# Optimization experiments

Measured on AMD Instinct MI355X. Metric: run time of the kernel, lower is better.

The kernel has to match this reference:

```python
import jax, jax.numpy as jnp
import numpy as np

B, N, K = 8, 1024, 16        # graphs, points per graph, kNN fan-in (loop=True includes self)
LATENT = 256
EPS = 1e-5                   # PyG BatchNorm eps


def _bn(x, g, b):
    # training-mode batch norm over all leading (node/edge) dims, per channel
    ax = tuple(range(x.ndim - 1))
    mu = jnp.mean(x, axis=ax, keepdims=True)
    var = jnp.var(x, axis=ax, keepdims=True)
    return g * (x - mu) * jax.lax.rsqrt(var + EPS) + b


def setup_inputs() -> dict:
    key = jax.random.key(0)
    ks = jax.random.split(key, 12)

    def lin(k, fi, fo):
        s = (6.0 / (fi + fo)) ** 0.5
        kw, kb = jax.random.split(k)
        W = jax.random.uniform(kw, (fi, fo), jnp.float32, -s, s)
        bb = jax.random.uniform(kb, (fo,), jnp.float32, -s, s)
        return W, bb

    pos = jax.random.normal(ks[0], (B * N, 3), jnp.float32)
    batch = jnp.repeat(jnp.arange(B, dtype=jnp.int32), N)

    c1_W1, c1_b1 = lin(ks[1], 6, 64)
    c1_W2, c1_b2 = lin(ks[2], 64, 64)
    c2_W1, c2_b1 = lin(ks[3], 67, 64)
    c2_W2, c2_b2 = lin(ks[4], 64, 128)
    c2_W3, c2_b3 = lin(ks[5], 128, 1024)
    lin_W, lin_b = lin(ks[6], 1024, LATENT)

    return {
        "pos": pos, "batch": batch,
        "c1_W1": c1_W1, "c1_b1": c1_b1,
        "c1_g1": jnp.ones((64,), jnp.float32), "c1_be1": jnp.zeros((64,), jnp.float32),
        "c1_W2": c1_W2, "c1_b2": c1_b2,
        "c2_W1": c2_W1, "c2_b1": c2_b1,
        "c2_g1": jnp.ones((64,), jnp.float32), "c2_be1": jnp.zeros((64,), jnp.float32),
        "c2_W2": c2_W2, "c2_b2": c2_b2,
        "c2_g2": jnp.ones((128,), jnp.float32), "c2_be2": jnp.zeros((128,), jnp.float32),
        "c2_W3": c2_W3, "c2_b3": c2_b3,
        "lin_W": lin_W, "lin_b": lin_b,
        "lin_g": jnp.ones((LATENT,), jnp.float32), "lin_be": jnp.zeros((LATENT,), jnp.float32),
    }


def reference(pos, batch,
              c1_W1, c1_b1, c1_g1, c1_be1, c1_W2, c1_b2,
              c2_W1, c2_b1, c2_g1, c2_be1, c2_W2, c2_b2,
              c2_g2, c2_be2, c2_W3, c2_b3,
              lin_W, lin_b, lin_g, lin_be):
    # ---- kNN graph (per-graph, loop=True: self is nearest) ----
    p3 = pos.reshape(B, N, 3)
    sq = jnp.sum(p3 * p3, axis=-1)                                   # [B,N]
    d = sq[:, :, None] + sq[:, None, :] - 2.0 * jnp.einsum('bnd,bmd->bnm', p3, p3)
    _, nbr = jax.lax.top_k(-d, K)                                    # [B,N,K] neighbor ids
    idx = (nbr + (jnp.arange(B) * N)[:, None, None]).reshape(B * N, K)

    # ---- PointNetConv 1: gather -> MLP([6,64,64]) -> max aggregate ----
    pj = pos[idx]                                                    # [P,K,3]
    rel = pj - pos[:, None, :]                                       # [P,K,3]
    feat = jnp.concatenate([pj, rel], axis=-1)                       # [P,K,6]
    h = jax.nn.relu(_bn(feat @ c1_W1 + c1_b1, c1_g1, c1_be1))
    x1 = jnp.max(h @ c1_W2 + c1_b2, axis=1)                          # [P,64]

    # ---- PointNetConv 2: MLP([67,64,128,1024]) -> max aggregate ----
    feat2 = jnp.concatenate([x1[idx], rel], axis=-1)                 # [P,K,67]
    h = jax.nn.relu(_bn(feat2 @ c2_W1 + c2_b1, c2_g1, c2_be1))
    h = jax.nn.relu(_bn(h @ c2_W2 + c2_b2, c2_g2, c2_be2))
    x2 = jnp.max(h @ c2_W3 + c2_b3, axis=1)                          # [P,1024]

    # ---- global max pool per graph + final MLP (plain_last=False) ----
    g = x2.reshape(B, N, -1).max(axis=1)                             # [B,1024]
    return jax.nn.relu(_bn(g @ lin_W + lin_b, lin_g, lin_be))        # [B,LATENT]
```

## Files before the change

### kernel.cpp

```cpp
#include <hip/hip_runtime.h>
#include <math.h>

#define NB   8
#define NPTS 1024
#define PTS  8192
#define KNN  16
#define PK   (PTS*KNN)

typedef __attribute__((ext_vector_type(8))) _Float16 f16x8;
typedef __attribute__((ext_vector_type(4))) float f32x4;

__device__ __forceinline__ unsigned short f2h(float f) {
  _Float16 h = (_Float16)f;
  union { _Float16 h; unsigned short u; } c; c.h = h;
  return c.u;
}
__device__ __forceinline__ float h2f(unsigned short u) {
  union { unsigned short u; _Float16 h; } c; c.u = u;
  return (float)c.h;
}

__global__ __launch_bounds__(256) void knn_conv1_kernel(const float* __restrict__ pos,
    const float* __restrict__ W1, const float* __restrict__ b1,
    int* __restrict__ idx, float* __restrict__ rel,
    unsigned short* __restrict__ z1h, float* __restrict__ mid1) {
  __shared__ float px[NPTS], py[NPTS], pz[NPTS];
  __shared__ float feat[4][KNN][6];
  __shared__ float ls[256], ls2[256];
  const int t = threadIdx.x;
  const int wv = t >> 6, lane = t & 63;
  const int b = blockIdx.x;
  const int graph = b >> 8;
  const int base = graph << 10;
  for (int j = t; j < NPTS; j += 256) {
    px[j] = pos[3*(base+j)];
    py[j] = pos[3*(base+j)+1];
    pz[j] = pos[3*(base+j)+2];
  }
  __syncthreads();

  const int il = ((b & 255) << 2) + wv;
  const int i  = base + il;
  const float pix = px[il], piy = py[il], piz = pz[il];
  const float sqi = pix*pix + piy*piy + piz*piz;

  unsigned long long key[16];
  #pragma unroll
  for (int q = 0; q < 16; ++q) {
    const int j = (q << 6) + lane;
    const float x = px[j], y = py[j], z = pz[j];
    const float sqj = x*x + y*y + z*z;
    const float dt  = pix*x + piy*y + piz*z;
    const float d   = sqi + sqj - 2.0f*dt;
    unsigned int db = __float_as_uint(d);
    db = (db >> 31) ? ~db : (db | 0x80000000u);
    key[q] = ((unsigned long long)db << 32) | (unsigned int)j;
  }

  #pragma unroll
  for (int k = 2; k <= 16; k <<= 1) {
    #pragma unroll
    for (int jj = k >> 1; jj > 0; jj >>= 1) {
      #pragma unroll
      for (int ii = 0; ii < 16; ++ii) {
        const int l = ii ^ jj;
        if (l > ii) {
          const bool up = ((ii & k) == 0);
          const unsigned long long a = key[ii], c = key[l];
          const bool sw = up ? (c < a) : (a < c);
          key[ii] = sw ? c : a;
          key[l]  = sw ? a : c;
        }
      }
    }
  }

  #pragma unroll
  for (int m = 1; m <= 32; m <<= 1) {
    unsigned long long pk[16];
    #pragma unroll
    for (int ii = 0; ii < 16; ++ii) pk[ii] = __shfl_xor(key[ii], m);
    #pragma unroll
    for (int ii = 0; ii < 16; ++ii) {
      const unsigned long long o = pk[15 - ii];
      key[ii] = (o < key[ii]) ? o : key[ii];
    }
    #pragma unroll
    for (int s = 8; s >= 1; s >>= 1) {
      #pragma unroll
      for (int ii = 0; ii < 16; ++ii) {
        if ((ii & s) == 0) {
          const unsigned long long a = key[ii], c = key[ii | s];
          key[ii]     = (c < a) ? c : a;
          key[ii | s] = (c < a) ? a : c;
        }
      }
    }
  }

  int selj = 0;
  #pragma unroll
  for (int s = 0; s < 16; ++s)
    if (lane == s) selj = (int)(key[s] & 1023u);

  if (lane < KNN) {
    const int r = i*KNN + lane;
    const float rx = px[selj] - pix, ry = py[selj] - piy, rz = pz[selj] - piz;
    idx[r] = base + selj;
    rel[3*r] = rx; rel[3*r+1] = ry; rel[3*r+2] = rz;
    feat[wv][lane][0] = px[selj]; feat[wv][lane][1] = py[selj]; feat[wv][lane][2] = pz[selj];
    feat[wv][lane][3] = rx;       feat[wv][lane][4] = ry;       feat[wv][lane][5] = rz;
  }

  float w[6];
  #pragma unroll
  for (int q = 0; q < 6; ++q) w[q] = W1[q*64 + lane];
  const float bb = b1[lane];
  float s = 0.0f, s2 = 0.0f;
  #pragma unroll
  for (int k = 0; k < KNN; ++k) {
    float z = bb;
    #pragma unroll
    for (int q = 0; q < 6; ++q) z += feat[wv][k][q]*w[q];
    z1h[(size_t)(i*KNN + k)*64 + lane] = f2h(z);
    s += z; s2 += z*z;
  }
  ls[t] = s; ls2[t] = s2;
  __syncthreads();
  if (t < 64) {
    float a  = ls[t] + ls[t+64] + ls[t+128] + ls[t+192];
    float a2 = ls2[t] + ls2[t+64] + ls2[t+128] + ls2[t+192];
    const int cp = (b & 7) * 128;
    atomicAdd(&mid1[cp + t], a);
    atomicAdd(&mid1[cp + 64 + t], a2);
  }
}

__global__ __launch_bounds__(256) void wprep_kernel(const float* __restrict__ W3,
    const float* __restrict__ W2, const float* __restrict__ W1c2,
    const float* __restrict__ W2c1,
    unsigned short* __restrict__ W3T, unsigned short* __restrict__ W2T,
    unsigned short* __restrict__ w1T, unsigned short* __restrict__ W2c1T) {
  const int b = blockIdx.x, t = threadIdx.x;
  if (b < 128) {
    const int k = b;
    const int ks = k >> 5, qd = (k >> 3) & 3, e = k & 7;
    for (int n = t; n < 1024; n += 256) {
      const int nb = n >> 4, mc = n & 15;
      W3T[((nb*4 + ks) << 9) + qd*128 + mc*8 + e] = f2h(W3[(size_t)k*1024 + n]);
    }
  } else if (b < 132) {
    for (int id = (b-128)*2048 + t; id < (b-127)*2048; id += 256) {
      const int n = id >> 6, k = id & 63;
      W2T[n*64 + k] = f2h(W2[k*128 + n]);
    }
  } else if (b < 136) {
    for (int id = (b-132)*1024 + t; id < (b-131)*1024; id += 256) {
      const int n = id >> 6, k = id & 63;
      w1T[n*64 + k] = f2h(W1c2[k*64 + n]);
    }
  } else {
    for (int id = (b-136)*1024 + t; id < (b-135)*1024; id += 256) {
      const int n = id >> 6, k = id & 63;
      W2c1T[n*64 + k] = f2h(W2c1[k*64 + n]);
    }
  }
}

__global__ __launch_bounds__(256) void conv1_l2max_mfma(
    const unsigned short* __restrict__ z1h, const float* __restrict__ mid1,
    const float* __restrict__ g1, const float* __restrict__ be1,
    const unsigned short* __restrict__ W2T, const float* __restrict__ b2,
    unsigned short* __restrict__ x1h) {
  __shared__ unsigned short As[128*64];
  __shared__ float scl[64], shl[64];
  const int r0 = blockIdx.x * 128;
  const int t = threadIdx.x;
  const int lane = t & 63, w = t >> 6;
  const int quad = lane >> 4, mcol = lane & 15;
  const float invR = 1.0f / (float)PK;

  if (t < 64) {
    float s = 0.0f, s2 = 0.0f;
    #pragma unroll
    for (int k = 0; k < 8; ++k) { s += mid1[k*128 + t]; s2 += mid1[k*128 + 64 + t]; }
    const float mu  = s * invR;
    const float var = s2 * invR - mu*mu;
    const float sc  = g1[t] * rsqrtf(var + 1e-5f);
    scl[t] = sc; shl[t] = be1[t] - mu*sc;
  }
  __syncthreads();

  {
    const int kb = t & 7, rr = t >> 3;
    float sc[8], sh[8];
    #pragma unroll
    for (int q = 0; q < 8; ++q) { sc[q] = scl[kb*8 + q]; sh[q] = shl[kb*8 + q]; }
    #pragma unroll
    for (int it = 0; it < 4; ++it) {
      const int r = rr + it*32;
      union { uint4 v; unsigned short s[8]; } in;
      in.v = *(const uint4*)(z1h + (size_t)(r0 + r)*64 + kb*8);
      union { unsigned short s[8]; uint4 v; } o;
      #pragma unroll
      for (int q = 0; q < 8; ++q)
        o.s[q] = f2h(fmaxf(h2f(in.s[q])*sc[q] + sh[q], 0.0f));
      *(uint4*)(As + r*64 + ((kb ^ (r & 7)) * 8)) = o.v;
    }
  }
  __syncthreads();

  const int wrow = (w >> 1) * 64;
  const int wncol = (w & 1) * 32;

  f32x4 acc[4][2];
  #pragma unroll
  for (int mi = 0; mi < 4; ++mi)
    #pragma unroll
    for (int ni = 0; ni < 2; ++ni)
      acc[mi][ni] = (f32x4){0.f, 0.f, 0.f, 0.f};

  #pragma unroll
  for (int ks = 0; ks < 2; ++ks) {
    f16x8 af[4], bfr[2];
    #pragma unroll
    for (int mi = 0; mi < 4; ++mi) {
      const int row = wrow + mi*16 + mcol;
      af[mi] = *(const f16x8*)(As + row*64 + (((ks*4 + quad) ^ (row & 7)) * 8));
    }
    #pragma unroll
    for (int ni = 0; ni < 2; ++ni) {
      const int nr = wncol + ni*16 + mcol;
      bfr[ni] = *(const f16x8*)(W2T + nr*64 + ks*32 + quad*8);
    }
    #pragma unroll
    for (int mi = 0; mi < 4; ++mi)
      #pragma unroll
      for (int ni = 0; ni < 2; ++ni)
        acc[mi][ni] = __builtin_amdgcn_mfma_f32_16x16x32_f16(af[mi], bfr[ni], acc[mi][ni], 0, 0, 0);
  }

  float bb[2];
  #pragma unroll
  for (int ni = 0; ni < 2; ++ni) bb[ni] = b2[wncol + ni*16 + mcol];
  #pragma unroll
  for (int mi = 0; mi < 4; ++mi) {
    const int p = blockIdx.x*8 + (w >> 1)*4 + mi;
    #pragma unroll
    for (int ni = 0; ni < 2; ++ni) {
      f32x4 a = acc[mi][ni];
      float m = fmaxf(fmaxf(a[0], a[1]), fmaxf(a[2], a[3]));
      m = fmaxf(m, __shfl_xor(m, 16));
      m = fmaxf(m, __shfl_xor(m, 32));
      if (quad == 0) x1h[(size_t)p*64 + wncol + ni*16 + mcol] = f2h(m + bb[ni]);
    }
  }
}

__global__ __launch_bounds__(256) void conv2_l1_mfma(
    const unsigned short* __restrict__ x1h, const int* __restrict__ idx,
    const float* __restrict__ rel, const unsigned short* __restrict__ w1T,
    const float* __restrict__ W1full, const float* __restrict__ b1,
    unsigned short* __restrict__ zah, float* __restrict__ midA) {
  __shared__ unsigned short S[128*64];
  __shared__ int   idxr[128];
  __shared__ float rl[128*3];
  __shared__ float ps[256];
  const int r0 = blockIdx.x * 128;
  const int t = threadIdx.x;
  const int lane = t & 63, w = t >> 6;
  const int quad = lane >> 4, mcol = lane & 15;

  if (t < 128) idxr[t] = idx[r0 + t];
  else if (t < 224) *(float4*)(rl + (t-128)*4) = *(const float4*)(rel + (size_t)r0*3 + (t-128)*4);
  __syncthreads();

  {
    const int kb = t & 7, rr = t >> 3;
    #pragma unroll
    for (int it = 0; it < 4; ++it) {
      const int r = rr + it*32;
      const int gj = idxr[r];
      const uint4 v = *(const uint4*)(x1h + (size_t)gj*64 + kb*8);
      *(uint4*)(S + r*64 + ((kb ^ (r & 7)) * 8)) = v;
    }
  }
  __syncthreads();

  const int wrow = (w >> 1) * 64;
  const int wcol = (w & 1) * 32;

  f16x8 af[2][4], bfr[2][2];
  #pragma unroll
  for (int ks = 0; ks < 2; ++ks)
    #pragma unroll
    for (int mi = 0; mi < 4; ++mi) {
      const int row = wrow + mi*16 + mcol;
      af[ks][mi] = *(const f16x8*)(S + row*64 + (((ks*4 + quad) ^ (row & 7)) * 8));
    }
  #pragma unroll
  for (int ks = 0; ks < 2; ++ks)
    #pragma unroll
    for (int ni = 0; ni < 2; ++ni) {
      const int nr = wcol + ni*16 + mcol;
      bfr[ks][ni] = *(const f16x8*)(w1T + nr*64 + ks*32 + quad*8);
    }

  f32x4 acc[4][2];
  #pragma unroll
  for (int mi = 0; mi < 4; ++mi)
    #pragma unroll
    for (int ni = 0; ni < 2; ++ni)
      acc[mi][ni] = (f32x4){0.f, 0.f, 0.f, 0.f};

  #pragma unroll
  for (int ks = 0; ks < 2; ++ks)
    #pragma unroll
    for (int mi = 0; mi < 4; ++mi)
      #pragma unroll
      for (int ni = 0; ni < 2; ++ni)
        acc[mi][ni] = __builtin_amdgcn_mfma_f32_16x16x32_f16(af[ks][mi], bfr[ks][ni], acc[mi][ni], 0, 0, 0);

  __syncthreads();

  float bb[2], wr0[2], wr1[2], wr2[2];
  #pragma unroll
  for (int ni = 0; ni < 2; ++ni) {
    const int col = wcol + ni*16 + mcol;
    bb[ni]  = b1[col];
    wr0[ni] = W1full[64*64 + col];
    wr1[ni] = W1full[65*64 + col];
    wr2[ni] = W1full[66*64 + col];
  }
  float s[2] = {0,0}, s2[2] = {0,0};
  #pragma unroll
  for (int mi = 0; mi < 4; ++mi) {
    #pragma unroll
    for (int j = 0; j < 4; ++j) {
      const int row = wrow + mi*16 + quad*4 + j;
      const float r0v = rl[row*3], r1v = rl[row*3+1], r2v = rl[row*3+2];
      #pragma unroll
      for (int ni = 0; ni < 2; ++ni) {
        const int col = wcol + ni*16 + mcol;
        const int g = col >> 3, o = col & 7;
        const float v = acc[mi][ni][j] + bb[ni] + r0v*wr0[ni] + r1v*wr1[ni] + r2v*wr2[ni];
        S[row*64 + ((g ^ (row & 7)) << 3) + o] = f2h(v);
        s[ni] += v; s2[ni] += v*v;
      }
    }
  }
  #pragma unroll
  for (int ni = 0; ni < 2; ++ni) {
    s[ni]  += __shfl_xor(s[ni], 16);  s[ni]  += __shfl_xor(s[ni], 32);
    s2[ni] += __shfl_xor(s2[ni], 16); s2[ni] += __shfl_xor(s2[ni], 32);
  }
  if (quad == 0) {
    const int rh = w >> 1;
    #pragma unroll
    for (int ni = 0; ni < 2; ++ni) {
      const int col = wcol + ni*16 + mcol;
      ps[rh*128 + col]      = s[ni];
      ps[rh*128 + 64 + col] = s2[ni];
    }
  }
  __syncthreads();

  #pragma unroll
  for (int i = 0; i < 4; ++i) {
    const int u = i*256 + t;
    const int row = u >> 3, gg = u & 7;
    *(uint4*)(zah + (size_t)(r0 + row)*64 + gg*8) =
        *(const uint4*)(S + row*64 + ((gg ^ (row & 7)) << 3));
  }
  if (t < 128) atomicAdd(&midA[(blockIdx.x & 7)*128 + t], ps[t] + ps[128 + t]);
}

__global__ __launch_bounds__(256) void conv2_l2_mfma(
    const unsigned short* __restrict__ zah, const float* __restrict__ midA,
    const float* __restrict__ g1, const float* __restrict__ be1,
    const unsigned short* __restrict__ W2T, const float* __restrict__ b2,
    unsigned short* __restrict__ zhb, float* __restrict__ midB) {
  __shared__ unsigned short S[128*128];
  __shared__ float ps[512];
  __shared__ float scl[64], shl[64];
  const int r0 = blockIdx.x * 128;
  const int t = threadIdx.x;
  const int lane = t & 63, w = t >> 6;
  const int quad = lane >> 4, mcol = lane & 15;
  const float invR = 1.0f / (float)PK;

  if (t < 64) {
    float s = 0.0f, s2 = 0.0f;
    #pragma unroll
    for (int k = 0; k < 8; ++k) { s += midA[k*128 + t]; s2 += midA[k*128 + 64 + t]; }
    const float mu  = s * invR;
    const float var = s2 * invR - mu*mu;
    const float sc  = g1[t] * rsqrtf(var + 1e-5f);
    scl[t] = sc; shl[t] = be1[t] - mu*sc;
  }
  __syncthreads();

  {
    const int kb = t & 7, rr = t >> 3;
    float sc[8], sh[8];
    #pragma unroll
    for (int q = 0; q < 8; ++q) { sc[q] = scl[kb*8 + q]; sh[q] = shl[kb*8 + q]; }
    #pragma unroll
    for (int it = 0; it < 4; ++it) {
      const int r = rr + it*32;
      union { uint4 v; unsigned short s[8]; } in;
      in.v = *(const uint4*)(zah + (size_t)(r0 + r)*64 + kb*8);
      union { unsigned short s[8]; uint4 v; } o;
      #pragma unroll
      for (int q = 0; q < 8; ++q)
        o.s[q] = f2h(fmaxf(h2f(in.s[q])*sc[q] + sh[q], 0.0f));
      *(uint4*)(S + r*64 + ((kb ^ (r & 7)) * 8)) = o.v;
    }
  }
  __syncthreads();

  const int wrow = (w >> 1) * 64;
  const int wcol = (w & 1) * 64;

  f16x8 af[2][4], bfr[2][4];
  #pragma unroll
  for (int ks = 0; ks < 2; ++ks)
    #pragma unroll
    for (int mi = 0; mi < 4; ++mi) {
      const int row = wrow + mi*16 + mcol;
      af[ks][mi] = *(const f16x8*)(S + row*64 + (((ks*4 + quad) ^ (row & 7)) * 8));
    }
  #pragma unroll
  for (int ks = 0; ks < 2; ++ks)
    #pragma unroll
    for (int ni = 0; ni < 4; ++ni) {
      const int nr = wcol + ni*16 + mcol;
      bfr[ks][ni] = *(const f16x8*)(W2T + nr*64 + ks*32 + quad*8);
    }

  f32x4 acc[4][4];
  #pragma unroll
  for (int mi = 0; mi < 4; ++mi)
    #pragma unroll
    for (int ni = 0; ni < 4; ++ni)
      acc[mi][ni] = (f32x4){0.f, 0.f, 0.f, 0.f};

  #pragma unroll
  for (int ks = 0; ks < 2; ++ks)
    #pragma unroll
    for (int mi = 0; mi < 4; ++mi)
      #pragma unroll
      for (int ni = 0; ni < 4; ++ni)
        acc[mi][ni] = __builtin_amdgcn_mfma_f32_16x16x32_f16(af[ks][mi], bfr[ks][ni], acc[mi][ni], 0, 0, 0);

  __syncthreads();

  float bb[4];
  #pragma unroll
  for (int ni = 0; ni < 4; ++ni) bb[ni] = b2[wcol + ni*16 + mcol];
  float s[4] = {0,0,0,0}, s2[4] = {0,0,0,0};
  #pragma unroll
  for (int mi = 0; mi < 4; ++mi) {
    #pragma unroll
    for (int ni = 0; ni < 4; ++ni) {
      const int col = wcol + ni*16 + mcol;
      const int g = col >> 3, o = col & 7;
      #pragma unroll
      for (int j = 0; j < 4; ++j) {
        const int row = wrow + mi*16 + quad*4 + j;
        const float v = acc[mi][ni][j] + bb[ni];
        S[row*128 + ((g ^ (row & 15)) << 3) + o] = f2h(v);
        s[ni] += v; s2[ni] += v*v;
      }
    }
  }
  #pragma unroll
  for (int ni = 0; ni < 4; ++ni) {
    s[ni]  += __shfl_xor(s[ni], 16);  s[ni]  += __shfl_xor(s[ni], 32);
    s2[ni] += __shfl_xor(s2[ni], 16); s2[ni] += __shfl_xor(s2[ni], 32);
  }
  if (quad == 0) {
    const int rh = w >> 1;
    #pragma unroll
    for (int ni = 0; ni < 4; ++ni) {
      const int col = wcol + ni*16 + mcol;
      ps[rh*256 + col]       = s[ni];
      ps[rh*256 + 128 + col] = s2[ni];
    }
  }
  __syncthreads();

  #pragma unroll
  for (int i = 0; i < 8; ++i) {
    const int u = i*256 + t;
    const int row = u >> 4, gg = u & 15;
    *(uint4*)(zhb + (size_t)(r0 + row)*128 + gg*8) =
        *(const uint4*)(S + row*128 + ((gg ^ (row & 15)) << 3));
  }
  atomicAdd(&midB[(blockIdx.x & 7)*256 + t], ps[t] + ps[256 + t]);
}

__global__ __launch_bounds__(256, 3) void conv2_l3max_mfma(
    const unsigned short* __restrict__ zhb, const float* __restrict__ midB,
    const float* __restrict__ g2, const float* __restrict__ be2,
    const unsigned short* __restrict__ W3T,
    float* __restrict__ pmax2) {
  __shared__ unsigned short As[128*128];
  __shared__ float pm[1024];
  __shared__ float scl[128], shl[128];
  const int rb = blockIdx.x & 1023, ch = blockIdx.x >> 10;
  const int r0 = rb * 128;
  const int t = threadIdx.x;
  const int lane = t & 63, w = t >> 6;
  const int quad = lane >> 4, mcol = lane & 15;
  const float invR = 1.0f / (float)PK;

  #pragma unroll
  for (int i = 0; i < 4; ++i) pm[i*256 + t] = -INFINITY;

  if (t < 128) {
    float s = 0.0f, s2 = 0.0f;
    #pragma unroll
    for (int k = 0; k < 8; ++k) { s += midB[k*256 + t]; s2 += midB[k*256 + 128 + t]; }
    const float mu  = s * invR;
    const float var = s2 * invR - mu*mu;
    const float sc  = g2[t] * rsqrtf(var + 1e-5f);
    scl[t] = sc; shl[t] = be2[t] - mu*sc;
  }
  __syncthreads();

  {
    const int kb = t & 15, rr = t >> 4;
    float sc[8], sh[8];
    #pragma unroll
    for (int q = 0; q < 8; ++q) { sc[q] = scl[kb*8 + q]; sh[q] = shl[kb*8 + q]; }
    #pragma unroll
    for (int it = 0; it < 8; ++it) {
      const int r = rr + it*16;
      union { uint4 v; unsigned short s[8]; } in;
      in.v = *(const uint4*)(zhb + (size_t)(r0 + r)*128 + kb*8);
      union { unsigned short s[8]; uint4 v; } o;
      #pragma unroll
      for (int q = 0; q < 8; ++q)
        o.s[q] = f2h(fmaxf(h2f(in.s[q])*sc[q] + sh[q], 0.0f));
      *(uint4*)(As + r*128 + ((kb ^ (r & 7)) * 8)) = o.v;
    }
  }
  __syncthreads();

  const int wrow = (w >> 1) * 64;
  const int wncol = (w & 1) * 32;
  const int rh = w >> 1;

  #pragma unroll 1
  for (int chunk = 0; chunk < 8; ++chunk) {
    const int nb0 = ch*32 + chunk*4 + (w & 1)*2;

    f32x4 acc[4][2];
    #pragma unroll
    for (int mi = 0; mi < 4; ++mi)
      #pragma unroll
      for (int ni = 0; ni < 2; ++ni)
        acc[mi][ni] = (f32x4){0.f, 0.f, 0.f, 0.f};

    #pragma unroll
    for (int ks = 0; ks < 4; ++ks) {
      f16x8 bfr[2], af[4];
      #pragma unroll
      for (int ni = 0; ni < 2; ++ni)
        bfr[ni] = *(const f16x8*)(W3T + (((nb0 + ni)*4 + ks) << 9) + lane*8);
      #pragma unroll
      for (int mi = 0; mi < 4; ++mi) {
        const int row = wrow + mi*16 + mcol;
        af[mi] = *(const f16x8*)(As + row*128 + (((ks*4 + quad) ^ (row & 7)) * 8));
      }
      #pragma unroll
      for (int mi = 0; mi < 4; ++mi)
        #pragma unroll
        for (int ni = 0; ni < 2; ++ni)
          acc[mi][ni] = __builtin_amdgcn_mfma_f32_16x16x32_f16(af[mi], bfr[ni], acc[mi][ni], 0, 0, 0);
    }

    #pragma unroll
    for (int ni = 0; ni < 2; ++ni) {
      float m4 = -INFINITY;
      #pragma unroll
      for (int mi = 0; mi < 4; ++mi) {
        f32x4 a = acc[mi][ni];
        m4 = fmaxf(m4, fmaxf(fmaxf(a[0], a[1]), fmaxf(a[2], a[3])));
      }
      m4 = fmaxf(m4, __shfl_xor(m4, 16));
      m4 = fmaxf(m4, __shfl_xor(m4, 32));
      if (quad == 0) {
        const int pc = rh*512 + chunk*64 + wncol + ni*16 + mcol;
        pm[pc] = fmaxf(pm[pc], m4);
      }
    }
  }
  __syncthreads();

  pmax2[(size_t)rb*1024 + ch*512 + t]       = fmaxf(pm[t], pm[512 + t]);
  pmax2[(size_t)rb*1024 + ch*512 + 256 + t] = fmaxf(pm[256 + t], pm[768 + t]);
}

__global__ __launch_bounds__(256) void pool_final_kernel(const float* __restrict__ pmax2,
    const float* __restrict__ b3, float* __restrict__ g) {
  const int b = blockIdx.x >> 2, q = blockIdx.x & 3;
  const int c = q*256 + threadIdx.x;
  const float* p = pmax2 + (size_t)b*128*1024 + c;
  float m = -INFINITY;
  for (int rb = 0; rb < 128; ++rb) m = fmaxf(m, p[(size_t)rb*1024]);
  g[b*1024 + c] = m + b3[c];
}

__global__ __launch_bounds__(256) void lin_kernel(const float* __restrict__ g,
    const float* __restrict__ W, float* __restrict__ zpart) {
  const int b = blockIdx.x >> 2, q = blockIdx.x & 3;
  const int o = threadIdx.x;
  const float* gb = g + b*1024 + q*256;
  const float* Wq = W + q*256*256;
  float acc = 0.0f;
  for (int c = 0; c < 256; ++c) acc += gb[c] * Wq[c*256 + o];
  zpart[blockIdx.x*256 + o] = acc;
}

__global__ __launch_bounds__(256) void final_kernel(const float* __restrict__ zpart,
    const float* __restrict__ lb, const float* __restrict__ lg,
    const float* __restrict__ lbe, float* __restrict__ out) {
  const int o = threadIdx.x;
  float z[NB]; float s = 0.0f, s2 = 0.0f;
  #pragma unroll
  for (int b = 0; b < NB; ++b) {
    float v = lb[o];
    #pragma unroll
    for (int q = 0; q < 4; ++q) v += zpart[(b*4+q)*256 + o];
    z[b] = v; s += v; s2 += v*v;
  }
  const float mu  = s * 0.125f;
  const float var = s2 * 0.125f - mu*mu;
  const float inv = rsqrtf(var + 1e-5f);
  const float sc = lg[o]*inv, sh = lbe[o] - mu*sc;
  #pragma unroll
  for (int b = 0; b < NB; ++b) out[b*256 + o] = fmaxf(z[b]*sc + sh, 0.0f);
}

extern "C" void kernel_launch(void* const* d_in, const int* in_sizes, int n_in,
                              void* d_out, int out_size, void* d_ws, size_t ws_size,
                              hipStream_t stream) {
  const float* pos    = (const float*)d_in[0];
  const float* c1_W1  = (const float*)d_in[2];
  const float* c1_b1  = (const float*)d_in[3];
  const float* c1_g1  = (const float*)d_in[4];
  const float* c1_be1 = (const float*)d_in[5];
  const float* c1_W2  = (const float*)d_in[6];
  const float* c1_b2  = (const float*)d_in[7];
  const float* c2_W1  = (const float*)d_in[8];
  const float* c2_b1  = (const float*)d_in[9];
  const float* c2_g1  = (const float*)d_in[10];
  const float* c2_be1 = (const float*)d_in[11];
  const float* c2_W2  = (const float*)d_in[12];
  const float* c2_b2  = (const float*)d_in[13];
  const float* c2_g2  = (const float*)d_in[14];
  const float* c2_be2 = (const float*)d_in[15];
  const float* c2_W3  = (const float*)d_in[16];
  const float* c2_b3  = (const float*)d_in[17];
  const float* lin_W  = (const float*)d_in[18];
  const float* lin_b  = (const float*)d_in[19];
  const float* lin_g  = (const float*)d_in[20];
  const float* lin_be = (const float*)d_in[21];
  float* out = (float*)d_out;

  char* ws = (char*)d_ws;
  int*   idx     = (int*)  (ws + 0);
  float* rel     = (float*)(ws + 524288);
  float* zpart   = (float*)(ws + 2097152 + 2048);
  float* gpool   = (float*)(ws + 2097152 + 2048 + 32768);
  float* mid1    = (float*)(ws + 2164736);
  float* midA    = (float*)(ws + 2164736 + 4096);
  float* midB    = (float*)(ws + 2164736 + 8192);
  unsigned short* W2T   = (unsigned short*)(ws + 2295808);
  unsigned short* w1T   = (unsigned short*)(ws + 2312192);
  unsigned short* W2c1T = (unsigned short*)(ws + 2320384);
  unsigned short* z1h = (unsigned short*)(ws + 2426880);
  unsigned short* zah = (unsigned short*)(ws + 2426880);
  float* pmax2   = (float*)(ws + 2426880);
  unsigned short* x1h = (unsigned short*)(ws + 35981312);
  unsigned short* zhb = (unsigned short*)(ws + 38078464);
  unsigned short* W3T = (unsigned short*)(ws + 71632896);

  hipMemsetAsync(ws + 2164736, 0, 16384, stream);
  wprep_kernel<<<140, 256, 0, stream>>>(c2_W3, c2_W2, c2_W1, c1_W2, W3T, W2T, w1T, W2c1T);
  knn_conv1_kernel<<<PTS/4, 256, 0, stream>>>(pos, c1_W1, c1_b1, idx, rel, z1h, mid1);
  conv1_l2max_mfma<<<PK/128, 256, 0, stream>>>(z1h, mid1, c1_g1, c1_be1, W2c1T, c1_b2, x1h);
  conv2_l1_mfma<<<PK/128, 256, 0, stream>>>(x1h, idx, rel, w1T, c2_W1, c2_b1, zah, midA);
  conv2_l2_mfma<<<PK/128, 256, 0, stream>>>(zah, midA, c2_g1, c2_be1, W2T, c2_b2, zhb, midB);
  conv2_l3max_mfma<<<PK/64, 256, 0, stream>>>(zhb, midB, c2_g2, c2_be2, W3T, pmax2);
  pool_final_kernel<<<NB*4, 256, 0, stream>>>(pmax2, c2_b3, gpool);
  lin_kernel<<<32, 256, 0, stream>>>(gpool, lin_W, zpart);
  final_kernel<<<1, 256, 0, stream>>>(zpart, lin_b, lin_g, lin_be, out);
}
```

Measured before the change: 251.5 us.

## Replace bitonic kNN sort with radix-select threshold search via ballots

Swaps the per-lane bitonic sort plus cross-lane merge network on 64-bit keys for a 32-step bitwise radix select. Each step counts candidates below a trial threshold with wave ballots. The neighbors below the threshold, plus ties up to 16, are then compacted into slots using mbcnt lane ranks. This removes many 64-bit compare-swaps and shuffles. In exchange, neighbors are no longer stored in sorted distance order and tie-breaking may differ, which is harmless here because the aggregation is a max.

```diff
diff --git a/kernel.cpp b/kernel.cpp
--- a/kernel.cpp
+++ b/kernel.cpp
@@ -18,6 +18,10 @@
 __device__ __forceinline__ float h2f(unsigned short u) {
   union { unsigned short u; _Float16 h; } c; c.u = u;
   return (float)c.h;
+}
+__device__ __forceinline__ int lanerank(unsigned long long m) {
+  return __builtin_amdgcn_mbcnt_hi((unsigned)(m >> 32),
+         __builtin_amdgcn_mbcnt_lo((unsigned)m, 0));
 }
 
 __global__ __launch_bounds__(256) void knn_conv1_kernel(const float* __restrict__ pos,
@@ -44,7 +48,7 @@
   const float pix = px[il], piy = py[il], piz = pz[il];
   const float sqi = pix*pix + piy*piy + piz*piz;
 
-  unsigned long long key[16];
+  unsigned key[16];
   #pragma unroll
   for (int q = 0; q < 16; ++q) {
     const int j = (q << 6) + lane;
@@ -52,74 +56,58 @@
     const float sqj = x*x + y*y + z*z;
     const float dt  = pix*x + piy*y + piz*z;
     const float d   = sqi + sqj - 2.0f*dt;
-    unsigned int db = __float_as_uint(d);
-    db = (db >> 31) ? ~db : (db | 0x80000000u);
-    key[q] = ((unsigned long long)db << 32) | (unsigned int)j;
-  }
-
-  #pragma unroll
-  for (int k = 2; k <= 16; k <<= 1) {
-    #pragma unroll
-    for (int jj = k >> 1; jj > 0; jj >>= 1) {
-      #pragma unroll
-      for (int ii = 0; ii < 16; ++ii) {
-        const int l = ii ^ jj;
-        if (l > ii) {
-          const bool up = ((ii & k) == 0);
-          const unsigned long long a = key[ii], c = key[l];
-          const bool sw = up ? (c < a) : (a < c);
-          key[ii] = sw ? c : a;
-          key[l]  = sw ? a : c;
-        }
-      }
-    }
-  }
-
-  #pragma unroll
-  for (int m = 1; m <= 32; m <<= 1) {
-    unsigned long long pk[16];
-    #pragma unroll
-    for (int ii = 0; ii < 16; ++ii) pk[ii] = __shfl_xor(key[ii], m);
-    #pragma unroll
-    for (int ii = 0; ii < 16; ++ii) {
-      const unsigned long long o = pk[15 - ii];
-      key[ii] = (o < key[ii]) ? o : key[ii];
-    }
-    #pragma unroll
-    for (int s = 8; s >= 1; s >>= 1) {
-      #pragma unroll
-      for (int ii = 0; ii < 16; ++ii) {
-        if ((ii & s) == 0) {
-          const unsigned long long a = key[ii], c = key[ii | s];
-          key[ii]     = (c < a) ? c : a;
-          key[ii | s] = (c < a) ? a : c;
-        }
-      }
-    }
-  }
-
-  int selj = 0;
-  #pragma unroll
-  for (int s = 0; s < 16; ++s)
-    if (lane == s) selj = (int)(key[s] & 1023u);
-
-  if (lane < KNN) {
-    const int r = i*KNN + lane;
-    const float rx = px[selj] - pix, ry = py[selj] - piy, rz = pz[selj] - piz;
-    idx[r] = base + selj;
-    rel[3*r] = rx; rel[3*r+1] = ry; rel[3*r+2] = rz;
-    feat[wv][lane][0] = px[selj]; feat[wv][lane][1] = py[selj]; feat[wv][lane][2] = pz[selj];
-    feat[wv][lane][3] = rx;       feat[wv][lane][4] = ry;       feat[wv][lane][5] = rz;
+    const unsigned db = __float_as_uint(d);
+    key[q] = (db >> 31) ? ~db : (db | 0x80000000u);
+  }
+
+  unsigned V = 0;
+  #pragma unroll 1
+  for (int bb = 31; bb >= 0; --bb) {
+    const unsigned test = V | (1u << bb);
+    int cnt = 0;
+    #pragma unroll
+    for (int q = 0; q < 16; ++q)
+      cnt += __popcll(__ballot(key[q] < test));
+    if (cnt < 16) V = test;
+  }
+
+  int c = 0;
+  #pragma unroll
+  for (int q = 0; q < 16; ++q)
+    c += __popcll(__ballot(key[q] < V));
+
+  int p_lt = 0, p_eq = c;
+  #pragma unroll 1
+  for (int q = 0; q < 16; ++q) {
+    const unsigned long long mlt = __ballot(key[q] < V);
+    const unsigned long long meq = __ballot(key[q] == V);
+    int slot = -1;
+    if (key[q] < V) slot = p_lt + lanerank(mlt);
+    else if (key[q] == V) {
+      const int s = p_eq + lanerank(meq);
+      if (s < 16) slot = s;
+    }
+    if (slot >= 0) {
+      const int j = (q << 6) + lane;
+      const int r = i*KNN + slot;
+      const float rx = px[j] - pix, ry = py[j] - piy, rz = pz[j] - piz;
+      idx[r] = base + j;
+      rel[3*r] = rx; rel[3*r+1] = ry; rel[3*r+2] = rz;
+      feat[wv][slot][0] = px[j]; feat[wv][slot][1] = py[j]; feat[wv][slot][2] = pz[j];
+      feat[wv][slot][3] = rx;    feat[wv][slot][4] = ry;    feat[wv][slot][5] = rz;
+    }
+    p_lt += __popcll(mlt);
+    p_eq += __popcll(meq);
   }
 
   float w[6];
   #pragma unroll
   for (int q = 0; q < 6; ++q) w[q] = W1[q*64 + lane];
-  const float bb = b1[lane];
+  const float bbv = b1[lane];
   float s = 0.0f, s2 = 0.0f;
   #pragma unroll
   for (int k = 0; k < KNN; ++k) {
-    float z = bb;
+    float z = bbv;
     #pragma unroll
     for (int q = 0; q < 6; ++q) z += feat[wv][k][q]*w[q];
     z1h[(size_t)(i*KNN + k)*64 + lane] = f2h(z);
```

Measured after the change: 236.0 us. 6.2% less time.
